# Kernel optimization log

Measured on AMD Instinct MI355X. Metric: run time of the kernel, lower is better.

The kernel has to match this reference:

```python
import jax, jax.numpy as jnp
import numpy as np

B, N, D, H = 4, 2048, 512, 8
DH = D // H
DFF = 4 * D
EPS = 1e-5


def layernorm(x, g, b):
    mu = jnp.mean(x, axis=-1, keepdims=True)
    var = jnp.mean((x - mu) ** 2, axis=-1, keepdims=True)
    return (x - mu) * jax.lax.rsqrt(var + EPS) * g + b


def setup_inputs() -> dict:
    key = jax.random.key(0)
    ks = jax.random.split(key, 8)
    s = 0.02
    return {
        "x": jax.random.normal(ks[0], (B, N, D), dtype=jnp.float32),
        "ln1_g": jnp.ones((D,), jnp.float32),
        "ln1_b": jnp.zeros((D,), jnp.float32),
        "Wqkv": jax.random.normal(ks[1], (D, 3 * D), jnp.float32) * s,
        "bqkv": jnp.zeros((3 * D,), jnp.float32),
        "Wproj": jax.random.normal(ks[2], (D, D), jnp.float32) * s,
        "bproj": jnp.zeros((D,), jnp.float32),
        "ln2_g": jnp.ones((D,), jnp.float32),
        "ln2_b": jnp.zeros((D,), jnp.float32),
        "W1": jax.random.normal(ks[3], (D, DFF), jnp.float32) * s,
        "b1": jnp.zeros((DFF,), jnp.float32),
        "W2": jax.random.normal(ks[4], (DFF, D), jnp.float32) * s,
        "b2": jnp.zeros((D,), jnp.float32),
    }


def reference(x, ln1_g, ln1_b, Wqkv, bqkv, Wproj, bproj, ln2_g, ln2_b, W1, b1, W2, b2):
    scale = DH ** -0.5
    # --- PreNorm + MHSA + residual ---
    h = layernorm(x, ln1_g, ln1_b)                      # [B,N,D]
    qkv = h @ Wqkv + bqkv                               # [B,N,3D]
    qkv = qkv.reshape(B, N, 3, H, DH)
    q, k, v = qkv[:, :, 0], qkv[:, :, 1], qkv[:, :, 2]  # [B,N,H,DH]
    attn = jnp.einsum("bnhd,bmhd->bhnm", q, k) * scale  # [B,H,N,N]
    attn = jax.nn.softmax(attn, axis=-1)
    out = jnp.einsum("bhnm,bmhd->bnhd", attn, v).reshape(B, N, D)
    x = x + out @ Wproj + bproj
    # --- PreNorm + GELU-MLP + residual ---
    h2 = layernorm(x, ln2_g, ln2_b)
    ff = jax.nn.gelu(h2 @ W1 + b1, approximate=False) @ W2 + b2
    return x + ff
```

## Files before the change

### kernel.cpp

```cpp
#include <hip/hip_runtime.h>

#define B_ 4
#define N_ 2048
#define D_ 512
#define H_ 8
#define DH_ 64
#define ROWS_ 8192
#define KSCALE 0.18033688011112042f

typedef float f32x4 __attribute__((ext_vector_type(4)));
typedef short short8v __attribute__((ext_vector_type(8)));
typedef short short4v __attribute__((ext_vector_type(4)));
typedef unsigned uint4v __attribute__((ext_vector_type(4)));

__device__ __forceinline__ short f2bf(float f) {
    unsigned u = __builtin_bit_cast(unsigned, f);
    u += 0x7FFFu + ((u >> 16) & 1u);
    return (short)(u >> 16);
}

__device__ __forceinline__ unsigned cvtpk_bf16(float lo, float hi) {
    unsigned r;
    asm("v_cvt_pk_bf16_f32 %0, %1, %2" : "=v"(r) : "v"(lo), "v"(hi));
    return r;
}

__device__ __forceinline__ void gload16(const void* g, void* l) {
    __builtin_amdgcn_global_load_lds(
        (const __attribute__((address_space(1))) unsigned int*)g,
        (__attribute__((address_space(3))) unsigned int*)l, 16, 0, 0);
}

__device__ __forceinline__ void waitvm0_barrier() {
    asm volatile("s_waitcnt vmcnt(0)" ::: "memory");
    __builtin_amdgcn_s_barrier();
}

__global__ __launch_bounds__(256) void ln_bf16_kernel(const float* __restrict__ x,
                                                      const float* __restrict__ g,
                                                      const float* __restrict__ bb,
                                                      short* __restrict__ out) {
    int wave = threadIdx.x >> 6;
    int lane = threadIdx.x & 63;
    int row  = blockIdx.x * 4 + wave;
    const float* xr = x + (size_t)row * D_;

    float4 v0 = ((const float4*)xr)[lane * 2 + 0];
    float4 v1 = ((const float4*)xr)[lane * 2 + 1];

    float s = v0.x + v0.y + v0.z + v0.w + v1.x + v1.y + v1.z + v1.w;
    #pragma unroll
    for (int off = 32; off; off >>= 1) s += __shfl_xor(s, off, 64);
    float mu = s * (1.0f / D_);

    float d0 = v0.x - mu, d1 = v0.y - mu, d2 = v0.z - mu, d3 = v0.w - mu;
    float d4 = v1.x - mu, d5 = v1.y - mu, d6 = v1.z - mu, d7 = v1.w - mu;
    float vs = d0*d0 + d1*d1 + d2*d2 + d3*d3 + d4*d4 + d5*d5 + d6*d6 + d7*d7;
    #pragma unroll
    for (int off = 32; off; off >>= 1) vs += __shfl_xor(vs, off, 64);
    float rstd = rsqrtf(vs * (1.0f / D_) + 1e-5f);

    float4 g0 = ((const float4*)g)[lane * 2 + 0];
    float4 g1 = ((const float4*)g)[lane * 2 + 1];
    float4 b0 = ((const float4*)bb)[lane * 2 + 0];
    float4 b1 = ((const float4*)bb)[lane * 2 + 1];

    short8v ov;
    ov[0] = f2bf(d0 * rstd * g0.x + b0.x);
    ov[1] = f2bf(d1 * rstd * g0.y + b0.y);
    ov[2] = f2bf(d2 * rstd * g0.z + b0.z);
    ov[3] = f2bf(d3 * rstd * g0.w + b0.w);
    ov[4] = f2bf(d4 * rstd * g1.x + b1.x);
    ov[5] = f2bf(d5 * rstd * g1.y + b1.y);
    ov[6] = f2bf(d6 * rstd * g1.z + b1.z);
    ov[7] = f2bf(d7 * rstd * g1.w + b1.w);
    *(short8v*)&out[(size_t)row * D_ + lane * 8] = ov;
}

__global__ __launch_bounds__(256) void wt_kernel(const float* __restrict__ W,
                                                 short* __restrict__ WT,
                                                 int K, int N) {
    __shared__ short Ts[64][72];
    int tid = threadIdx.x;
    int n0 = blockIdx.x * 64, k0 = blockIdx.y * 64;

    #pragma unroll
    for (int i = 0; i < 4; ++i) {
        int idx = tid + i * 256;
        int k = idx >> 4, nq = (idx & 15) * 4;
        float4 wv = *(const float4*)&W[(size_t)(k0 + k) * N + n0 + nq];
        short4v t;
        t[0] = f2bf(wv.x); t[1] = f2bf(wv.y); t[2] = f2bf(wv.z); t[3] = f2bf(wv.w);
        *(short4v*)&Ts[k][nq] = t;
    }
    __syncthreads();

    int n = tid >> 2, kq = (tid & 3) * 16;
    short8v o0, o1;
    #pragma unroll
    for (int j = 0; j < 8; ++j) { o0[j] = Ts[kq + j][n]; o1[j] = Ts[kq + 8 + j][n]; }
    *(short8v*)&WT[(size_t)(n0 + n) * K + k0 + kq]     = o0;
    *(short8v*)&WT[(size_t)(n0 + n) * K + k0 + kq + 8] = o1;
}

template<bool GELU, bool RESID, bool OUTBF, bool QKVMODE>
__global__ __launch_bounds__(256) void gemm_bf16(const short* __restrict__ A,
                                                 const short* __restrict__ BT,
                                                 const float* __restrict__ bias,
                                                 const float* __restrict__ resid,
                                                 float* __restrict__ Cf,
                                                 short* __restrict__ Cb,
                                                 short* __restrict__ vtg,
                                                 int M, int N, int K) {
    __shared__ short As[2][8192];
    __shared__ short Bs[2][4096];
    int tid = threadIdx.x;
    int l = tid & 63, w = tid >> 6;
    int wr = w >> 1, wc = w & 1;
    int l15 = l & 15, lg = l >> 4;
    int row0 = blockIdx.x * 128, col0 = blockIdx.y * 64;

    int rsub = l >> 3;
    int kq_  = ((l & 7) ^ rsub) * 8;
    int rsw  = l15 & 7;

    const short* ap[4];
    const short* bp[2];
    #pragma unroll
    for (int i = 0; i < 4; ++i)
        ap[i] = A + (size_t)(row0 + i * 32 + w * 8 + rsub) * K + kq_;
    bp[0] = BT + (size_t)(col0 + w * 8 + rsub) * K + kq_;
    bp[1] = BT + (size_t)(col0 + 32 + w * 8 + rsub) * K + kq_;

    int aoff0 = (wr * 64 + l15) * 64 + ((lg ^ rsw)) * 8;
    int aoff1 = (wr * 64 + l15) * 64 + (((4 + lg) ^ rsw)) * 8;
    int boff0 = (wc * 32 + l15) * 64 + ((lg ^ rsw)) * 8;
    int boff1 = (wc * 32 + l15) * 64 + (((4 + lg) ^ rsw)) * 8;

    const f32x4 zero4 = {0.f, 0.f, 0.f, 0.f};
    f32x4 acc[4][2];
    #pragma unroll
    for (int m = 0; m < 4; ++m)
        #pragma unroll
        for (int n = 0; n < 2; ++n) acc[m][n] = zero4;

    auto stage = [&](int bf) {
        #pragma unroll
        for (int i = 0; i < 4; ++i) {
            gload16(ap[i], &As[bf][(i * 4 + w) * 512]);
            ap[i] += 64;
        }
        gload16(bp[0], &Bs[bf][w * 512]);       bp[0] += 64;
        gload16(bp[1], &Bs[bf][(4 + w) * 512]); bp[1] += 64;
    };

    auto compute = [&](int bf) {
        #pragma unroll
        for (int ks = 0; ks < 2; ++ks) {
            short8v a[4], bfr[2];
            #pragma unroll
            for (int m = 0; m < 4; ++m)
                a[m] = *(const short8v*)&As[bf][(ks ? aoff1 : aoff0) + m * 1024];
            #pragma unroll
            for (int n = 0; n < 2; ++n)
                bfr[n] = *(const short8v*)&Bs[bf][(ks ? boff1 : boff0) + n * 1024];
            __builtin_amdgcn_s_setprio(1);
            #pragma unroll
            for (int m = 0; m < 4; ++m)
                #pragma unroll
                for (int n = 0; n < 2; ++n)
                    acc[m][n] = __builtin_amdgcn_mfma_f32_16x16x32_bf16(a[m], bfr[n], acc[m][n], 0, 0, 0);
            __builtin_amdgcn_s_setprio(0);
        }
    };

    stage(0);
    waitvm0_barrier();

    int NH = K >> 7;
    for (int t2 = 0; t2 < NH; ++t2) {
        stage(1);
        compute(0);
        waitvm0_barrier();
        if (t2 + 1 < NH) stage(0);
        compute(1);
        waitvm0_barrier();
    }

    if (QKVMODE && col0 >= 1024) {
        int b = row0 >> 11;
        int nb = row0 & 2047;
        #pragma unroll
        for (int n = 0; n < 2; ++n) {
            int col = col0 + wc * 32 + n * 16 + l15;
            float bv = bias[col];
            int hd = col - 1024;
            size_t vrow = (size_t)(b * 512 + hd) * N_;
            #pragma unroll
            for (int m = 0; m < 4; ++m) {
                int nbase = nb + wr * 64 + m * 16 + lg * 4;
                uint2 uu;
                uu.x = cvtpk_bf16(acc[m][n][0] + bv, acc[m][n][1] + bv);
                uu.y = cvtpk_bf16(acc[m][n][2] + bv, acc[m][n][3] + bv);
                *(uint2*)&vtg[vrow + nbase] = uu;
            }
        }
        return;
    }

    float qscl = (QKVMODE && col0 < 512) ? KSCALE : 1.0f;
    #pragma unroll
    for (int n = 0; n < 2; ++n) {
        int col = col0 + wc * 32 + n * 16 + l15;
        float bv = bias[col];
        #pragma unroll
        for (int m = 0; m < 4; ++m) {
            #pragma unroll
            for (int i = 0; i < 4; ++i) {
                int row = row0 + wr * 64 + m * 16 + lg * 4 + i;
                size_t off = (size_t)row * N + col;
                float v = acc[m][n][i] + bv;
                if (RESID) v += resid[off];
                if (GELU)  v = 0.5f * v * (1.0f + erff(v * 0.70710678118654752f));
                if (QKVMODE) v *= qscl;
                if (OUTBF) Cb[off] = f2bf(v);
                else       Cf[off] = v;
            }
        }
    }
}

__global__ __launch_bounds__(256) void fattn_bf16(const short* __restrict__ qkvb,
                                                  const short* __restrict__ vtg,
                                                  short* __restrict__ attnout) {
    __shared__ short Ks[2][4096];
    __shared__ short Vt[2][4096];

    int tid = threadIdx.x;
    int l = tid & 63, w = tid >> 6;
    int l15 = l & 15, lg = l >> 4;
    int bh = blockIdx.x, qt = blockIdx.y;
    int b = bh >> 3, h = bh & 7;
    int n0 = qt * 128;
    int qb = w * 32;

    int hK = ((l15 >> 2) << 1) | (l15 & 1);
    int hV = l15 & 7;
    int kperm = ((l15 >> 2) << 3) + (l15 & 3);

    int koff0 = kperm * 64 + (lg ^ hK) * 8;
    int koff1 = kperm * 64 + (((4 + lg) ^ hK)) * 8;
    int voff0 = l15 * 64 + (lg ^ hV) * 8;
    int voff1 = l15 * 64 + (((4 + lg) ^ hV)) * 8;

    short8v bQ[2][2];
    #pragma unroll
    for (int qi = 0; qi < 2; ++qi)
        #pragma unroll
        for (int ks = 0; ks < 2; ++ks)
            bQ[qi][ks] = *(const short8v*)
                &qkvb[(size_t)(b * N_ + n0 + qb + qi * 16 + l15) * 1536 + h * 64 + ks * 32 + lg * 8];

    short8v ones;
    #pragma unroll
    for (int j = 0; j < 8; ++j) ones[j] = (short)0x3F80;

    const f32x4 zero4 = {0.f, 0.f, 0.f, 0.f};
    f32x4 o[2][4], l_acc[2];
    #pragma unroll
    for (int qi = 0; qi < 2; ++qi) {
        l_acc[qi] = zero4;
        #pragma unroll
        for (int df = 0; df < 4; ++df) o[qi][df] = zero4;
    }

    int lr = l >> 3, lc = l & 7;
    const short* kp[2];
    const short* vp[2];
    #pragma unroll
    for (int i = 0; i < 2; ++i) {
        int g = w * 2 + i, r = g * 8 + lr;
        int hKs = ((g & 3) << 1) | (lr & 1);
        kp[i] = &qkvb[(size_t)(b * N_ + r) * 1536 + 512 + h * 64 + ((lc ^ hKs) << 3)];
        vp[i] = &vtg[((size_t)bh * 64 + r) * N_ + ((lc ^ lr) << 3)];
    }

    auto stage = [&](int bf) {
        #pragma unroll
        for (int i = 0; i < 2; ++i) {
            int g = w * 2 + i;
            gload16(kp[i], &Ks[bf][g * 512]); kp[i] += 64 * 1536;
            gload16(vp[i], &Vt[bf][g * 512]); vp[i] += 64;
        }
    };

    auto compute = [&](int bf) {
        f32x4 s[2][4];
        #pragma unroll
        for (int kf = 0; kf < 4; ++kf) {
            short8v aK0 = *(const short8v*)&Ks[bf][koff0 + (kf >> 1) * 2048 + (kf & 1) * 256];
            short8v aK1 = *(const short8v*)&Ks[bf][koff1 + (kf >> 1) * 2048 + (kf & 1) * 256];
            __builtin_amdgcn_s_setprio(1);
            #pragma unroll
            for (int qi = 0; qi < 2; ++qi) {
                s[qi][kf] = __builtin_amdgcn_mfma_f32_16x16x32_bf16(aK0, bQ[qi][0], zero4, 0, 0, 0);
                s[qi][kf] = __builtin_amdgcn_mfma_f32_16x16x32_bf16(aK1, bQ[qi][1], s[qi][kf], 0, 0, 0);
            }
            __builtin_amdgcn_s_setprio(0);
        }

        short8v bP[2][2];
        #pragma unroll
        for (int qi = 0; qi < 2; ++qi) {
            #pragma unroll
            for (int kf = 0; kf < 4; ++kf)
                #pragma unroll
                for (int i = 0; i < 4; ++i)
                    s[qi][kf][i] = exp2f(s[qi][kf][i]);
            #pragma unroll
            for (int ks = 0; ks < 2; ++ks) {
                uint4v u;
                u[0] = cvtpk_bf16(s[qi][2 * ks][0],     s[qi][2 * ks][1]);
                u[1] = cvtpk_bf16(s[qi][2 * ks][2],     s[qi][2 * ks][3]);
                u[2] = cvtpk_bf16(s[qi][2 * ks + 1][0], s[qi][2 * ks + 1][1]);
                u[3] = cvtpk_bf16(s[qi][2 * ks + 1][2], s[qi][2 * ks + 1][3]);
                bP[qi][ks] = __builtin_bit_cast(short8v, u);
            }
        }

        __builtin_amdgcn_s_setprio(1);
        #pragma unroll
        for (int qi = 0; qi < 2; ++qi) {
            l_acc[qi] = __builtin_amdgcn_mfma_f32_16x16x32_bf16(ones, bP[qi][0], l_acc[qi], 0, 0, 0);
            l_acc[qi] = __builtin_amdgcn_mfma_f32_16x16x32_bf16(ones, bP[qi][1], l_acc[qi], 0, 0, 0);
        }
        __builtin_amdgcn_s_setprio(0);
        #pragma unroll
        for (int df = 0; df < 4; ++df) {
            short8v aV0 = *(const short8v*)&Vt[bf][voff0 + df * 1024];
            short8v aV1 = *(const short8v*)&Vt[bf][voff1 + df * 1024];
            __builtin_amdgcn_s_setprio(1);
            #pragma unroll
            for (int qi = 0; qi < 2; ++qi) {
                o[qi][df] = __builtin_amdgcn_mfma_f32_16x16x32_bf16(aV0, bP[qi][0], o[qi][df], 0, 0, 0);
                o[qi][df] = __builtin_amdgcn_mfma_f32_16x16x32_bf16(aV1, bP[qi][1], o[qi][df], 0, 0, 0);
            }
            __builtin_amdgcn_s_setprio(0);
        }
    };

    stage(0);
    waitvm0_barrier();

    for (int t2 = 0; t2 < 16; ++t2) {
        stage(1);
        compute(0);
        waitvm0_barrier();
        if (t2 + 1 < 16) stage(0);
        compute(1);
        waitvm0_barrier();
    }

    #pragma unroll
    for (int qi = 0; qi < 2; ++qi) {
        float linv = 1.0f / l_acc[qi][0];
        size_t rowb = (size_t)(b * N_ + n0 + qb + qi * 16 + l15) * D_ + h * 64;
        #pragma unroll
        for (int df = 0; df < 4; ++df) {
            uint2 uu;
            uu.x = cvtpk_bf16(o[qi][df][0] * linv, o[qi][df][1] * linv);
            uu.y = cvtpk_bf16(o[qi][df][2] * linv, o[qi][df][3] * linv);
            *(uint2*)&attnout[rowb + df * 16 + lg * 4] = uu;
        }
    }
}

extern "C" void kernel_launch(void* const* d_in, const int* in_sizes, int n_in,
                              void* d_out, int out_size, void* d_ws, size_t ws_size,
                              hipStream_t stream) {
    const float* x      = (const float*)d_in[0];
    const float* ln1_g  = (const float*)d_in[1];
    const float* ln1_b  = (const float*)d_in[2];
    const float* Wqkv   = (const float*)d_in[3];
    const float* bqkv   = (const float*)d_in[4];
    const float* Wproj  = (const float*)d_in[5];
    const float* bproj  = (const float*)d_in[6];
    const float* ln2_g  = (const float*)d_in[7];
    const float* ln2_b  = (const float*)d_in[8];
    const float* W1     = (const float*)d_in[9];
    const float* b1     = (const float*)d_in[10];
    const float* W2     = (const float*)d_in[11];
    const float* b2     = (const float*)d_in[12];
    float* out = (float*)d_out;

    char* ws = (char*)d_ws;
    short* h_bf    = (short*)(ws + (size_t)0);
    short* qkv_bf  = (short*)(ws + ((size_t)8  << 20));
    short* vtg     = (short*)(ws + ((size_t)32 << 20));
    short* attn_bf = (short*)(ws + ((size_t)40 << 20));
    float* x2      = (float*)(ws + ((size_t)48 << 20));
    short* h2_bf   = (short*)(ws + ((size_t)64 << 20));
    short* ffh_bf  = (short*)(ws + ((size_t)72 << 20));
    short* WTqkv   = (short*)(ws + ((size_t)104 << 20));
    short* WTproj  = (short*)(ws + ((size_t)106 << 20));
    short* WT1     = (short*)(ws + ((size_t)108 << 20));
    short* WT2     = (short*)(ws + ((size_t)110 << 20));

    dim3 blk(256);

    wt_kernel<<<dim3(24, 8),  blk, 0, stream>>>(Wqkv,  WTqkv,  512,  1536);
    wt_kernel<<<dim3(8, 8),   blk, 0, stream>>>(Wproj, WTproj, 512,  512);
    wt_kernel<<<dim3(32, 8),  blk, 0, stream>>>(W1,    WT1,    512,  2048);
    wt_kernel<<<dim3(8, 32),  blk, 0, stream>>>(W2,    WT2,    2048, 512);

    ln_bf16_kernel<<<ROWS_ / 4, blk, 0, stream>>>(x, ln1_g, ln1_b, h_bf);

    gemm_bf16<false, false, true, true><<<dim3(64, 24), blk, 0, stream>>>(
        h_bf, WTqkv, bqkv, nullptr, nullptr, qkv_bf, vtg, ROWS_, 1536, 512);

    fattn_bf16<<<dim3(32, 16), blk, 0, stream>>>(qkv_bf, vtg, attn_bf);

    gemm_bf16<false, true, false, false><<<dim3(64, 8), blk, 0, stream>>>(
        attn_bf, WTproj, bproj, x, x2, nullptr, nullptr, ROWS_, 512, 512);

    ln_bf16_kernel<<<ROWS_ / 4, blk, 0, stream>>>(x2, ln2_g, ln2_b, h2_bf);

    gemm_bf16<true, false, true, false><<<dim3(64, 32), blk, 0, stream>>>(
        h2_bf, WT1, b1, nullptr, nullptr, ffh_bf, nullptr, ROWS_, 2048, 512);

    gemm_bf16<false, true, false, false><<<dim3(64, 8), blk, 0, stream>>>(
        ffh_bf, WT2, b2, x2, out, nullptr, nullptr, ROWS_, 512, 2048);
}
```

Baseline: 177.7 us.

## Triple-buffer GEMM LDS staging with partial vmcnt waits

Switches the bf16 GEMM main loop from double to triple buffering in LDS. Two tiles are kept in flight, and it waits only for the oldest group of global-to-LDS loads (vmcnt 6) rather than draining all of them before each barrier. This is meant to hide global load latency behind MFMA compute. In exchange LDS use grows by half, to 72KB per block, which may reduce occupancy.

```diff
diff --git a/kernel.cpp b/kernel.cpp
--- a/kernel.cpp
+++ b/kernel.cpp
@@ -12,6 +12,8 @@
 typedef short short8v __attribute__((ext_vector_type(8)));
 typedef short short4v __attribute__((ext_vector_type(4)));
 typedef unsigned uint4v __attribute__((ext_vector_type(4)));
+
+#define WAITVM(N) asm volatile("s_waitcnt vmcnt(" #N ")" ::: "memory")
 
 __device__ __forceinline__ short f2bf(float f) {
     unsigned u = __builtin_bit_cast(unsigned, f);
@@ -112,8 +114,8 @@
                                                  short* __restrict__ Cb,
                                                  short* __restrict__ vtg,
                                                  int M, int N, int K) {
-    __shared__ short As[2][8192];
-    __shared__ short Bs[2][4096];
+    __shared__ short As[3][8192];
+    __shared__ short Bs[3][4096];
     int tid = threadIdx.x;
     int l = tid & 63, w = tid >> 6;
     int wr = w >> 1, wc = w & 1;
@@ -155,15 +157,17 @@
     };
 
     auto compute = [&](int bf) {
+        const short* Ab = As[bf];
+        const short* Bb = Bs[bf];
         #pragma unroll
         for (int ks = 0; ks < 2; ++ks) {
             short8v a[4], bfr[2];
             #pragma unroll
             for (int m = 0; m < 4; ++m)
-                a[m] = *(const short8v*)&As[bf][(ks ? aoff1 : aoff0) + m * 1024];
+                a[m] = *(const short8v*)&Ab[(ks ? aoff1 : aoff0) + m * 1024];
             #pragma unroll
             for (int n = 0; n < 2; ++n)
-                bfr[n] = *(const short8v*)&Bs[bf][(ks ? boff1 : boff0) + n * 1024];
+                bfr[n] = *(const short8v*)&Bb[(ks ? boff1 : boff0) + n * 1024];
             __builtin_amdgcn_s_setprio(1);
             #pragma unroll
             for (int m = 0; m < 4; ++m)
@@ -174,17 +178,25 @@
         }
     };
 
+    int NT = K >> 6;
     stage(0);
-    waitvm0_barrier();
-
-    int NH = K >> 7;
-    for (int t2 = 0; t2 < NH; ++t2) {
-        stage(1);
-        compute(0);
-        waitvm0_barrier();
-        if (t2 + 1 < NH) stage(0);
-        compute(1);
-        waitvm0_barrier();
+    stage(1);
+    WAITVM(6);
+    __builtin_amdgcn_s_barrier();
+
+    int cb = 0, sb = 2;
+    for (int t = 0; t < NT; ++t) {
+        if (t + 2 < NT) {
+            stage(sb);
+            compute(cb);
+            WAITVM(6);
+        } else {
+            compute(cb);
+            WAITVM(0);
+        }
+        __builtin_amdgcn_s_barrier();
+        cb = (cb == 2) ? 0 : cb + 1;
+        sb = (sb == 2) ? 0 : sb + 1;
     }
 
     if (QKVMODE && col0 >= 1024) {
```

New measurement: 205.9 us. 1.16x slower.
